# Performance work log

Hardware: AMD Instinct MI355X
Metric: run time of the kernel (lower is better)

Reference implementation:

```python
import jax, jax.numpy as jnp
import numpy as np

B, T, I, H, O = 4096, 256, 16, 32, 1


def setup_inputs() -> dict:
    key = jax.random.key(0)
    ks = jax.random.split(key, 8)
    s_ih = 1.0 / np.sqrt(H)
    x = jax.random.normal(ks[0], (B, T, I), dtype=jnp.float32)
    # PyTorch nn.LSTM params: gate order [i, f, g, o], uniform(-1/sqrt(H), 1/sqrt(H))
    W_ih = jax.random.uniform(ks[1], (4 * H, I), minval=-s_ih, maxval=s_ih, dtype=jnp.float32)
    W_hh = jax.random.uniform(ks[2], (4 * H, H), minval=-s_ih, maxval=s_ih, dtype=jnp.float32)
    b_ih = jax.random.uniform(ks[3], (4 * H,), minval=-s_ih, maxval=s_ih, dtype=jnp.float32)
    b_hh = jax.random.uniform(ks[4], (4 * H,), minval=-s_ih, maxval=s_ih, dtype=jnp.float32)
    W_fc = jax.random.uniform(ks[5], (O, H), minval=-s_ih, maxval=s_ih, dtype=jnp.float32)
    b_fc = jax.random.uniform(ks[6], (O,), minval=-s_ih, maxval=s_ih, dtype=jnp.float32)
    return {"x": x, "W_ih": W_ih, "W_hh": W_hh, "b_ih": b_ih, "b_hh": b_hh,
            "W_fc": W_fc, "b_fc": b_fc}


def _lstm_last_hidden(x, W_ih, W_hh, b_ih, b_hh):
    # Precompute input contributions for all timesteps: [T, B, 4H]
    xg = (jnp.einsum('bti,gi->btg', x, W_ih) + b_ih + b_hh).transpose(1, 0, 2)
    h0 = jnp.zeros((x.shape[0], W_hh.shape[1]), dtype=x.dtype)
    c0 = jnp.zeros_like(h0)

    def step(carry, xg_t):
        h, c = carry
        gates = xg_t + h @ W_hh.T  # [B, 4H]
        i, f, g, o = jnp.split(gates, 4, axis=-1)
        i = jax.nn.sigmoid(i)
        f = jax.nn.sigmoid(f)
        g = jnp.tanh(g)
        o = jax.nn.sigmoid(o)
        c = f * c + i * g
        h = o * jnp.tanh(c)
        return (h, c), None

    (h_last, _), _ = jax.lax.scan(step, (h0, c0), xg)
    return h_last


def reference(x, W_ih, W_hh, b_ih, b_hh, W_fc, b_fc):
    h_last = _lstm_last_hidden(x, W_ih, W_hh, b_ih, b_hh)
    # Dropout is identity in eval mode
    return h_last @ W_fc.T + b_fc  # [B, O]
```

## Files before the change

kernel.cpp:

```cpp
#include <hip/hip_runtime.h>

#define B_ 4096
#define T_ 256
#define I_ 16
#define H_ 32

__device__ __forceinline__ float sigm_(float x) {
    float e = __expf(-x);
    return __builtin_amdgcn_rcpf(1.0f + e);
}
__device__ __forceinline__ float tanh_(float x) {
    float e = __expf(-2.0f * x);
    float r = __builtin_amdgcn_rcpf(1.0f + e);
    return __fmaf_rn(2.0f, r, -1.0f);
}

__global__ __launch_bounds__(64, 2)
void lstm_fused_kernel(const float* __restrict__ x,
                       const float* __restrict__ Wih,
                       const float* __restrict__ Whh,
                       const float* __restrict__ bih,
                       const float* __restrict__ bhh,
                       const float* __restrict__ Wfc,
                       const float* __restrict__ bfc,
                       float* __restrict__ out)
{
    __shared__ __align__(16) float hbuf[2][H_];
    __shared__ __align__(16) float xbuf[2][8 * I_];

    const int tid  = threadIdx.x;
    const int elem = tid >> 5;
    const int idx  = tid & 31;
    const int b    = blockIdx.x * 2 + elem;

    float wih[4][I_];
    float whh[4][H_];
    float bias[4];
#pragma unroll
    for (int q = 0; q < 4; ++q) {
        const int row = q * 32 + idx;
#pragma unroll
        for (int k4 = 0; k4 < I_ / 4; ++k4) {
            const float4 v = *reinterpret_cast<const float4*>(Wih + row * I_ + k4 * 4);
            wih[q][k4 * 4 + 0] = v.x; wih[q][k4 * 4 + 1] = v.y;
            wih[q][k4 * 4 + 2] = v.z; wih[q][k4 * 4 + 3] = v.w;
        }
#pragma unroll
        for (int j4 = 0; j4 < H_ / 4; ++j4) {
            const float4 v = *reinterpret_cast<const float4*>(Whh + row * H_ + j4 * 4);
            whh[q][j4 * 4 + 0] = v.x; whh[q][j4 * 4 + 1] = v.y;
            whh[q][j4 * 4 + 2] = v.z; whh[q][j4 * 4 + 3] = v.w;
        }
        bias[q] = bih[row] + bhh[row];
    }

    hbuf[elem][idx] = 0.0f;
    float c  = 0.0f;
    float hj = 0.0f;
    __syncthreads();

    const float* xb = x + (size_t)b * (T_ * I_);
    float4 xnext = *reinterpret_cast<const float4*>(xb + idx * 4);

    for (int tb = 0; tb < T_ / 8; ++tb) {
        *reinterpret_cast<float4*>(&xbuf[elem][idx * 4]) = xnext;
        if (tb + 1 < T_ / 8) {
            xnext = *reinterpret_cast<const float4*>(xb + (tb + 1) * (8 * I_) + idx * 4);
        }
        __syncthreads();

#pragma unroll
        for (int tt = 0; tt < 8; ++tt) {
            float ai = bias[0], af = bias[1], ag = bias[2], ao = bias[3];

            const float* xt = &xbuf[elem][tt * I_];
#pragma unroll
            for (int k4 = 0; k4 < I_ / 4; ++k4) {
                const float4 xv = *reinterpret_cast<const float4*>(xt + k4 * 4);
                const float xs0 = xv.x, xs1 = xv.y, xs2 = xv.z, xs3 = xv.w;
                ai = __fmaf_rn(xs0, wih[0][k4 * 4 + 0], ai);
                af = __fmaf_rn(xs0, wih[1][k4 * 4 + 0], af);
                ag = __fmaf_rn(xs0, wih[2][k4 * 4 + 0], ag);
                ao = __fmaf_rn(xs0, wih[3][k4 * 4 + 0], ao);
                ai = __fmaf_rn(xs1, wih[0][k4 * 4 + 1], ai);
                af = __fmaf_rn(xs1, wih[1][k4 * 4 + 1], af);
                ag = __fmaf_rn(xs1, wih[2][k4 * 4 + 1], ag);
                ao = __fmaf_rn(xs1, wih[3][k4 * 4 + 1], ao);
                ai = __fmaf_rn(xs2, wih[0][k4 * 4 + 2], ai);
                af = __fmaf_rn(xs2, wih[1][k4 * 4 + 2], af);
                ag = __fmaf_rn(xs2, wih[2][k4 * 4 + 2], ag);
                ao = __fmaf_rn(xs2, wih[3][k4 * 4 + 2], ao);
                ai = __fmaf_rn(xs3, wih[0][k4 * 4 + 3], ai);
                af = __fmaf_rn(xs3, wih[1][k4 * 4 + 3], af);
                ag = __fmaf_rn(xs3, wih[2][k4 * 4 + 3], ag);
                ao = __fmaf_rn(xs3, wih[3][k4 * 4 + 3], ao);
            }

#pragma unroll
            for (int j4 = 0; j4 < H_ / 4; ++j4) {
                const float4 hv = *reinterpret_cast<const float4*>(&hbuf[elem][j4 * 4]);
                const float h0 = hv.x, h1 = hv.y, h2 = hv.z, h3 = hv.w;
                ai = __fmaf_rn(h0, whh[0][j4 * 4 + 0], ai);
                af = __fmaf_rn(h0, whh[1][j4 * 4 + 0], af);
                ag = __fmaf_rn(h0, whh[2][j4 * 4 + 0], ag);
                ao = __fmaf_rn(h0, whh[3][j4 * 4 + 0], ao);
                ai = __fmaf_rn(h1, whh[0][j4 * 4 + 1], ai);
                af = __fmaf_rn(h1, whh[1][j4 * 4 + 1], af);
                ag = __fmaf_rn(h1, whh[2][j4 * 4 + 1], ag);
                ao = __fmaf_rn(h1, whh[3][j4 * 4 + 1], ao);
                ai = __fmaf_rn(h2, whh[0][j4 * 4 + 2], ai);
                af = __fmaf_rn(h2, whh[1][j4 * 4 + 2], af);
                ag = __fmaf_rn(h2, whh[2][j4 * 4 + 2], ag);
                ao = __fmaf_rn(h2, whh[3][j4 * 4 + 2], ao);
                ai = __fmaf_rn(h3, whh[0][j4 * 4 + 3], ai);
                af = __fmaf_rn(h3, whh[1][j4 * 4 + 3], af);
                ag = __fmaf_rn(h3, whh[2][j4 * 4 + 3], ag);
                ao = __fmaf_rn(h3, whh[3][j4 * 4 + 3], ao);
            }

            const float gi = sigm_(ai);
            const float gf = sigm_(af);
            const float gg = tanh_(ag);
            const float go = sigm_(ao);

            c  = __fmaf_rn(gf, c, gi * gg);
            hj = go * tanh_(c);

            hbuf[elem][idx] = hj;
            __syncthreads();
        }
    }

    float p = hj * Wfc[idx];
#pragma unroll
    for (int off = 16; off > 0; off >>= 1) {
        p += __shfl_down(p, off, 32);
    }
    if (idx == 0) {
        out[b] = p + bfc[0];
    }
}

extern "C" void kernel_launch(void* const* d_in, const int* in_sizes, int n_in,
                              void* d_out, int out_size, void* d_ws, size_t ws_size,
                              hipStream_t stream) {
    const float* x   = (const float*)d_in[0];
    const float* Wih = (const float*)d_in[1];
    const float* Whh = (const float*)d_in[2];
    const float* bih = (const float*)d_in[3];
    const float* bhh = (const float*)d_in[4];
    const float* Wfc = (const float*)d_in[5];
    const float* bfc = (const float*)d_in[6];
    float* out = (float*)d_out;

    dim3 grid(B_ / 2);
    dim3 block(64);
    hipLaunchKernelGGL(lstm_fused_kernel, grid, block, 0, stream,
                       x, Wih, Whh, bih, bhh, Wfc, bfc, out);
}
```

Before: 271.4 us.

## Use packed fp16 dot2 for LSTM gate matvecs with fp32 accumulation

Converts weights, inputs and the shared hidden state to fp16 and computes the gate preactivations with v_dot2_f32_f16, which accumulates into fp32. This halves the number of multiply-add instructions, shrinks the weight register footprint so launch bounds can request more waves per SIMD, and halves LDS traffic for h and x. It also swaps __expf for a direct exp2 builtin. The cost is reduced precision in weights, inputs and the recurrent hidden state, and rounding error can build up over the 256 time steps.

Result: faster. 239.6 us (-11.7%).

```diff
diff --git a/kernel.cpp b/kernel.cpp
--- a/kernel.cpp
+++ b/kernel.cpp
@@ -5,56 +5,67 @@
 #define I_ 16
 #define H_ 32
 
+typedef _Float16 half2_t __attribute__((ext_vector_type(2)));
+typedef _Float16 half4_t __attribute__((ext_vector_type(4)));
+typedef _Float16 half8_t __attribute__((ext_vector_type(8)));
+
+union H8 {
+    half8_t v;
+    half2_t h[4];
+};
+
 __device__ __forceinline__ float sigm_(float x) {
-    float e = __expf(-x);
+    float e = __builtin_amdgcn_exp2f(-1.442695041f * x);
     return __builtin_amdgcn_rcpf(1.0f + e);
 }
 __device__ __forceinline__ float tanh_(float x) {
-    float e = __expf(-2.0f * x);
+    float e = __builtin_amdgcn_exp2f(-2.885390082f * x);
     float r = __builtin_amdgcn_rcpf(1.0f + e);
     return __fmaf_rn(2.0f, r, -1.0f);
 }
 
-__global__ __launch_bounds__(64, 2)
-void lstm_fused_kernel(const float* __restrict__ x,
-                       const float* __restrict__ Wih,
-                       const float* __restrict__ Whh,
-                       const float* __restrict__ bih,
-                       const float* __restrict__ bhh,
-                       const float* __restrict__ Wfc,
-                       const float* __restrict__ bfc,
-                       float* __restrict__ out)
+__global__ __launch_bounds__(64, 4)
+void lstm_fused_f16(const float* __restrict__ x,
+                    const float* __restrict__ Wih,
+                    const float* __restrict__ Whh,
+                    const float* __restrict__ bih,
+                    const float* __restrict__ bhh,
+                    const float* __restrict__ Wfc,
+                    const float* __restrict__ bfc,
+                    float* __restrict__ out)
 {
-    __shared__ __align__(16) float hbuf[2][H_];
-    __shared__ __align__(16) float xbuf[2][8 * I_];
+    __shared__ __align__(16) _Float16 hbuf[2][H_];
+    __shared__ __align__(16) _Float16 xbuf[2][8 * I_];
 
     const int tid  = threadIdx.x;
     const int elem = tid >> 5;
     const int idx  = tid & 31;
     const int b    = blockIdx.x * 2 + elem;
 
-    float wih[4][I_];
-    float whh[4][H_];
+    half2_t wih2[4][I_ / 2];
+    half2_t whh2[4][H_ / 2];
     float bias[4];
 #pragma unroll
     for (int q = 0; q < 4; ++q) {
         const int row = q * 32 + idx;
+        const float4* pih = reinterpret_cast<const float4*>(Wih + row * I_);
 #pragma unroll
-        for (int k4 = 0; k4 < I_ / 4; ++k4) {
-            const float4 v = *reinterpret_cast<const float4*>(Wih + row * I_ + k4 * 4);
-            wih[q][k4 * 4 + 0] = v.x; wih[q][k4 * 4 + 1] = v.y;
-            wih[q][k4 * 4 + 2] = v.z; wih[q][k4 * 4 + 3] = v.w;
+        for (int k = 0; k < I_ / 4; ++k) {
+            const float4 v = pih[k];
+            wih2[q][2 * k + 0] = half2_t{(_Float16)v.x, (_Float16)v.y};
+            wih2[q][2 * k + 1] = half2_t{(_Float16)v.z, (_Float16)v.w};
         }
+        const float4* phh = reinterpret_cast<const float4*>(Whh + row * H_);
 #pragma unroll
-        for (int j4 = 0; j4 < H_ / 4; ++j4) {
-            const float4 v = *reinterpret_cast<const float4*>(Whh + row * H_ + j4 * 4);
-            whh[q][j4 * 4 + 0] = v.x; whh[q][j4 * 4 + 1] = v.y;
-            whh[q][j4 * 4 + 2] = v.z; whh[q][j4 * 4 + 3] = v.w;
+        for (int k = 0; k < H_ / 4; ++k) {
+            const float4 v = phh[k];
+            whh2[q][2 * k + 0] = half2_t{(_Float16)v.x, (_Float16)v.y};
+            whh2[q][2 * k + 1] = half2_t{(_Float16)v.z, (_Float16)v.w};
         }
         bias[q] = bih[row] + bhh[row];
     }
 
-    hbuf[elem][idx] = 0.0f;
+    hbuf[elem][idx] = (_Float16)0.0f;
     float c  = 0.0f;
     float hj = 0.0f;
     __syncthreads();
@@ -63,7 +74,10 @@
     float4 xnext = *reinterpret_cast<const float4*>(xb + idx * 4);
 
     for (int tb = 0; tb < T_ / 8; ++tb) {
-        *reinterpret_cast<float4*>(&xbuf[elem][idx * 4]) = xnext;
+        half4_t xs;
+        xs[0] = (_Float16)xnext.x; xs[1] = (_Float16)xnext.y;
+        xs[2] = (_Float16)xnext.z; xs[3] = (_Float16)xnext.w;
+        *reinterpret_cast<half4_t*>(&xbuf[elem][idx * 4]) = xs;
         if (tb + 1 < T_ / 8) {
             xnext = *reinterpret_cast<const float4*>(xb + (tb + 1) * (8 * I_) + idx * 4);
         }
@@ -73,49 +87,36 @@
         for (int tt = 0; tt < 8; ++tt) {
             float ai = bias[0], af = bias[1], ag = bias[2], ao = bias[3];
 
-            const float* xt = &xbuf[elem][tt * I_];
+            H8 xv0, xv1;
+            xv0.v = *reinterpret_cast<const half8_t*>(&xbuf[elem][tt * I_]);
+            xv1.v = *reinterpret_cast<const half8_t*>(&xbuf[elem][tt * I_ + 8]);
 #pragma unroll
-            for (int k4 = 0; k4 < I_ / 4; ++k4) {
-                const float4 xv = *reinterpret_cast<const float4*>(xt + k4 * 4);
-                const float xs0 = xv.x, xs1 = xv.y, xs2 = xv.z, xs3 = xv.w;
-                ai = __fmaf_rn(xs0, wih[0][k4 * 4 + 0], ai);
-                af = __fmaf_rn(xs0, wih[1][k4 * 4 + 0], af);
-                ag = __fmaf_rn(xs0, wih[2][k4 * 4 + 0], ag);
-                ao = __fmaf_rn(xs0, wih[3][k4 * 4 + 0], ao);
-                ai = __fmaf_rn(xs1, wih[0][k4 * 4 + 1], ai);
-                af = __fmaf_rn(xs1, wih[1][k4 * 4 + 1], af);
-                ag = __fmaf_rn(xs1, wih[2][k4 * 4 + 1], ag);
-                ao = __fmaf_rn(xs1, wih[3][k4 * 4 + 1], ao);
-                ai = __fmaf_rn(xs2, wih[0][k4 * 4 + 2], ai);
-                af = __fmaf_rn(xs2, wih[1][k4 * 4 + 2], af);
-                ag = __fmaf_rn(xs2, wih[2][k4 * 4 + 2], ag);
-                ao = __fmaf_rn(xs2, wih[3][k4 * 4 + 2], ao);
-                ai = __fmaf_rn(xs3, wih[0][k4 * 4 + 3], ai);
-                af = __fmaf_rn(xs3, wih[1][k4 * 4 + 3], af);
-                ag = __fmaf_rn(xs3, wih[2][k4 * 4 + 3], ag);
-                ao = __fmaf_rn(xs3, wih[3][k4 * 4 + 3], ao);
+            for (int k = 0; k < 4; ++k) {
+                ai = __builtin_amdgcn_fdot2(xv0.h[k], wih2[0][k], ai, false);
+                af = __builtin_amdgcn_fdot2(xv0.h[k], wih2[1][k], af, false);
+                ag = __builtin_amdgcn_fdot2(xv0.h[k], wih2[2][k], ag, false);
+                ao = __builtin_amdgcn_fdot2(xv0.h[k], wih2[3][k], ao, false);
+            }
+#pragma unroll
+            for (int k = 0; k < 4; ++k) {
+                ai = __builtin_amdgcn_fdot2(xv1.h[k], wih2[0][4 + k], ai, false);
+                af = __builtin_amdgcn_fdot2(xv1.h[k], wih2[1][4 + k], af, false);
+                ag = __builtin_amdgcn_fdot2(xv1.h[k], wih2[2][4 + k], ag, false);
+                ao = __builtin_amdgcn_fdot2(xv1.h[k], wih2[3][4 + k], ao, false);
             }
 
 #pragma unroll
-            for (int j4 = 0; j4 < H_ / 4; ++j4) {
-                const float4 hv = *reinterpret_cast<const float4*>(&hbuf[elem][j4 * 4]);
-                const float h0 = hv.x, h1 = hv.y, h2 = hv.z, h3 = hv.w;
-                ai = __fmaf_rn(h0, whh[0][j4 * 4 + 0], ai);
-                af = __fmaf_rn(h0, whh[1][j4 * 4 + 0], af);
-                ag = __fmaf_rn(h0, whh[2][j4 * 4 + 0], ag);
-                ao = __fmaf_rn(h0, whh[3][j4 * 4 + 0], ao);
-                ai = __fmaf_rn(h1, whh[0][j4 * 4 + 1], ai);
-                af = __fmaf_rn(h1, whh[1][j4 * 4 + 1], af);
-                ag = __fmaf_rn(h1, whh[2][j4 * 4 + 1], ag);
-                ao = __fmaf_rn(h1, whh[3][j4 * 4 + 1], ao);
-                ai = __fmaf_rn(h2, whh[0][j4 * 4 + 2], ai);
-                af = __fmaf_rn(h2, whh[1][j4 * 4 + 2], af);
-                ag = __fmaf_rn(h2, whh[2][j4 * 4 + 2], ag);
-                ao = __fmaf_rn(h2, whh[3][j4 * 4 + 2], ao);
-                ai = __fmaf_rn(h3, whh[0][j4 * 4 + 3], ai);
-                af = __fmaf_rn(h3, whh[1][j4 * 4 + 3], af);
-                ag = __fmaf_rn(h3, whh[2][j4 * 4 + 3], ag);
-                ao = __fmaf_rn(h3, whh[3][j4 * 4 + 3], ao);
+            for (int j8 = 0; j8 < 4; ++j8) {
+                H8 hv;
+                hv.v = *reinterpret_cast<const half8_t*>(&hbuf[elem][j8 * 8]);
+#pragma unroll
+                for (int k = 0; k < 4; ++k) {
+                    const int p = j8 * 4 + k;
+                    ai = __builtin_amdgcn_fdot2(hv.h[k], whh2[0][p], ai, false);
+                    af = __builtin_amdgcn_fdot2(hv.h[k], whh2[1][p], af, false);
+                    ag = __builtin_amdgcn_fdot2(hv.h[k], whh2[2][p], ag, false);
+                    ao = __builtin_amdgcn_fdot2(hv.h[k], whh2[3][p], ao, false);
+                }
             }
 
             const float gi = sigm_(ai);
@@ -126,7 +127,7 @@
             c  = __fmaf_rn(gf, c, gi * gg);
             hj = go * tanh_(c);
 
-            hbuf[elem][idx] = hj;
+            hbuf[elem][idx] = (_Float16)hj;
             __syncthreads();
         }
     }
@@ -155,6 +156,6 @@
 
     dim3 grid(B_ / 2);
     dim3 block(64);
-    hipLaunchKernelGGL(lstm_fused_kernel, grid, block, 0, stream,
+    hipLaunchKernelGGL(lstm_fused_f16, grid, block, 0, stream,
                        x, Wih, Whh, bih, bhh, Wfc, bfc, out);
 }
```
